# Kernel tuning notes

Measured on AMD Instinct MI355X. Metric: run time of the kernel, lower is better.

## Reference

```python
import jax, jax.numpy as jnp
import numpy as np

N = 10000   # num_nodes (batch=1)
E = 160000  # num edges
CIN, H, T, OUT, K = 32, 64, 12, 12, 3


def _conv1d(x, w, b, pad):
    # x: [N, C_in, T], w: [C_out, C_in, K]
    out = jax.lax.conv_general_dilated(
        x, w, window_strides=(1,), padding=[(pad, pad)],
        dimension_numbers=('NCH', 'OIH', 'NCH'))
    return out + b[None, :, None]


def _gated_tconv(x, w, b):
    # GatedTemporalConv (dropout = identity in eval)
    out = _conv1d(x, w, b, K // 2)
    P, Q = jnp.split(out, 2, axis=1)
    return P * jax.nn.sigmoid(Q)


def _gcn(x, W, b, src, dst, ew):
    # PyG GCNConv, vectorized over all T timesteps in one fused pass.
    # x: [N, C_in, T], W: [C_out, C_in]
    xt = jnp.einsum('nct,oc->not', x, W)
    loop = jnp.arange(N)
    srcl = jnp.concatenate([src, loop])
    dstl = jnp.concatenate([dst, loop])
    ewl = jnp.concatenate([ew, jnp.ones((N,), ew.dtype)])
    deg = jax.ops.segment_sum(ewl, dstl, num_segments=N)
    dis = jnp.where(deg > 0, jax.lax.rsqrt(deg), 0.0)
    norm = dis[srcl] * ewl * dis[dstl]                      # [E+N]
    msg = xt[srcl] * norm[:, None, None]                    # [E+N, C_out, T]
    out = jax.ops.segment_sum(msg, dstl, num_segments=N)    # [N, C_out, T]
    return out + b[None, :, None]


def setup_inputs() -> dict:
    key = jax.random.key(0)
    ks = jax.random.split(key, 20)
    rn = lambda k, s: jax.random.normal(k, s, jnp.float32) * 0.05
    return {
        'x': jax.random.normal(ks[0], (N, CIN, T), jnp.float32),
        'edge_index': jax.random.randint(ks[1], (2, E), 0, N),
        'edge_weight': jax.random.uniform(ks[2], (E,), jnp.float32),
        'tc1a_w': rn(ks[3], (2 * H, CIN, K)), 'tc1a_b': rn(ks[4], (2 * H,)),
        'gc1_w': rn(ks[5], (H, H)),           'gc1_b': rn(ks[6], (H,)),
        'tc1b_w': rn(ks[7], (2 * H, H, K)),   'tc1b_b': rn(ks[8], (2 * H,)),
        'tc2a_w': rn(ks[9], (2 * H, H, K)),   'tc2a_b': rn(ks[10], (2 * H,)),
        'gc2_w': rn(ks[11], (H, H)),          'gc2_b': rn(ks[12], (H,)),
        'tc2b_w': rn(ks[13], (2 * H, H, K)),  'tc2b_b': rn(ks[14], (2 * H,)),
        'fin_w': rn(ks[15], (OUT, H, T)),     'fin_b': rn(ks[16], (OUT,)),
    }


def reference(x, edge_index, edge_weight,
              tc1a_w, tc1a_b, gc1_w, gc1_b, tc1b_w, tc1b_b,
              tc2a_w, tc2a_b, gc2_w, gc2_b, tc2b_w, tc2b_b,
              fin_w, fin_b):
    src, dst = edge_index[0], edge_index[1]
    h = _gated_tconv(x, tc1a_w, tc1a_b)
    h = jax.nn.relu(_gcn(h, gc1_w, gc1_b, src, dst, edge_weight))
    h = _gated_tconv(h, tc1b_w, tc1b_b)
    h = _gated_tconv(h, tc2a_w, tc2a_b)
    h = jax.nn.relu(_gcn(h, gc2_w, gc2_b, src, dst, edge_weight))
    h = _gated_tconv(h, tc2b_w, tc2b_b)
    h = _conv1d(h, fin_w, fin_b, 0)          # [N, OUT, 1] (kernel == T)
    h = h[:, :, 0]                            # squeeze(-1)
    return h.reshape(1, N, OUT)               # batch_size = 1
```

## Files before the change

kernel.cpp:

```cpp
#include <hip/hip_runtime.h>
#include <hip/hip_bf16.h>
#include <stdint.h>

#define N_NODES 10000
#define N_EDGES 160000

typedef unsigned short u16;
typedef unsigned int u32;
typedef short s16v8 __attribute__((ext_vector_type(8)));
typedef float f32v4 __attribute__((ext_vector_type(4)));

__device__ __forceinline__ float bf2f(u16 v){ return __uint_as_float(((u32)v) << 16); }
__device__ __forceinline__ u16 f2bf(float f){
    u32 u = __float_as_uint(f);
    u32 r = (u + 0x7fffu + ((u >> 16) & 1u)) >> 16;
    return (u16)r;
}

struct SmallPtrs { const void* p[14]; };

__device__ __constant__ const int g_seg_off[15] = {
    0, 12288, 12416, 16512, 16576, 41152, 41280,
    65856, 65984, 70080, 70144, 94720, 94848, 104064, 104076
};
__device__ __constant__ const int g_seg_kind[14] = {
    1, 0, 0, 0, 2, 0, 2, 0, 0, 0, 2, 0, 0, 0
};

__global__ void k_convert_init(SmallPtrs ps, u16* __restrict__ dst,
                               float* deg, int* cnt, int* cur){
    int i = blockIdx.x * blockDim.x + threadIdx.x;
    if (i < 104076){
        int seg = 0, base = 0;
#pragma unroll
        for (int s = 0; s < 14; s++){
            if (i >= g_seg_off[s]){ seg = s; base = g_seg_off[s]; }
        }
        int li = i - base;
        float v = ((const float*)ps.p[seg])[li];
        int kind = g_seg_kind[seg];
        int dsto = li;
        if (kind){
            int CIN = (kind == 1) ? 32 : 64;
            int o = li / (3 * CIN);
            int rem = li - o * (3 * CIN);
            int c = rem / 3, d = rem - c * 3;
            dsto = d * 128 * CIN + o * CIN + c;
        }
        dst[base + dsto] = f2bf(v);
    }
    if (i < N_NODES){ deg[i] = 1.0f; cnt[i] = 0; cur[i] = 0; }
}

__launch_bounds__(256, 2)
__global__ void k_gconv_count(const float* __restrict__ xin, const u16* __restrict__ wg,
                              const u16* __restrict__ bg, u16* __restrict__ out,
                              const int* __restrict__ ei, const float* __restrict__ ew,
                              float* deg, int* cnt){
    if (blockIdx.x >= 1250){
        int e = (blockIdx.x - 1250) * 256 + threadIdx.x;
        if (e < N_EDGES){
            int d = ei[N_EDGES + e];
            atomicAdd(&deg[d], ew[e]);
            atomicAdd(&cnt[d], 1);
        }
        return;
    }
    __shared__ __attribute__((aligned(16))) u16 xT[8][14][40];
    __shared__ __attribute__((aligned(16))) u16 Ho[8][12][72];
    int tid = threadIdx.x;
    int n0 = blockIdx.x * 8;

    for (int i = tid; i < 8 * 40; i += 256){
        int g = i / 40, c = i % 40;
        xT[g][0][c] = 0; xT[g][13][c] = 0;
    }
    {
        int g = tid >> 5, c = tid & 31;
        const float4* p = (const float4*)(xin + ((size_t)(n0 + g) * 32 + c) * 12);
        float4 v0 = p[0], v1 = p[1], v2 = p[2];
        xT[g][1][c] = f2bf(v0.x);  xT[g][2][c] = f2bf(v0.y);
        xT[g][3][c] = f2bf(v0.z);  xT[g][4][c] = f2bf(v0.w);
        xT[g][5][c] = f2bf(v1.x);  xT[g][6][c] = f2bf(v1.y);
        xT[g][7][c] = f2bf(v1.z);  xT[g][8][c] = f2bf(v1.w);
        xT[g][9][c] = f2bf(v2.x);  xT[g][10][c] = f2bf(v2.y);
        xT[g][11][c] = f2bf(v2.z); xT[g][12][c] = f2bf(v2.w);
    }
    int lane = tid & 63, wave = tid >> 6;
    int col = lane & 15, quad = lane >> 4;
    int o_p = wave * 16 + col, o_q = o_p + 64;

    s16v8 Bf[3][2];
#pragma unroll
    for (int pq = 0; pq < 2; pq++){
        int o = pq ? o_q : o_p;
#pragma unroll
        for (int d = 0; d < 3; d++)
            Bf[d][pq] = *(const s16v8*)(wg + d * 4096 + o * 32 + quad * 8);
    }
    __syncthreads();

    f32v4 aP[6], aQ[6];
#pragma unroll
    for (int mt = 0; mt < 6; mt++){ aP[mt] = (f32v4)0.f; aQ[mt] = (f32v4)0.f; }
#pragma unroll
    for (int mt = 0; mt < 6; mt++){
        int m = mt * 16 + col;
        int g = m / 12, t = m - 12 * g;
#pragma unroll
        for (int d = 0; d < 3; d++){
            s16v8 a = *(const s16v8*)&xT[g][t + d][quad * 8];
            aP[mt] = __builtin_amdgcn_mfma_f32_16x16x32_bf16(a, Bf[d][0], aP[mt], 0, 0, 0);
            aQ[mt] = __builtin_amdgcn_mfma_f32_16x16x32_bf16(a, Bf[d][1], aQ[mt], 0, 0, 0);
        }
    }
    float bP = bf2f(bg[o_p]), bQ = bf2f(bg[o_q]);
#pragma unroll
    for (int mt = 0; mt < 6; mt++){
#pragma unroll
        for (int r = 0; r < 4; r++){
            int m2 = mt * 16 + quad * 4 + r;
            int g = m2 / 12, t = m2 - 12 * g;
            float pv = aP[mt][r] + bP, qv = aQ[mt][r] + bQ;
            Ho[g][t][o_p] = f2bf(pv / (1.f + __expf(-qv)));
        }
    }
    __syncthreads();
    for (int i = tid; i < 768; i += 256){
        int g = i / 96, r = i % 96, t = r / 8, ch = r % 8;
        *(s16v8*)(out + (size_t)(n0 + g) * 768 + t * 64 + ch * 8) = *(const s16v8*)&Ho[g][t][ch * 8];
    }
}

__global__ void k_scan_dis(const int* __restrict__ cnt, int* __restrict__ off,
                           const float* __restrict__ deg, float* __restrict__ dis){
    __shared__ int wsum[16], woff[16];
    int t = threadIdx.x;
    int lane = t & 63, wv = t >> 6;
    int base = t * 10;
    int loc[10];
    int mysum = 0;
    if (base < N_NODES){
#pragma unroll
        for (int j = 0; j < 10; j++){ loc[j] = mysum; mysum += cnt[base + j]; }
    }
    int s = mysum;
#pragma unroll
    for (int d = 1; d < 64; d <<= 1){
        int v = __shfl_up(s, d, 64);
        if (lane >= d) s += v;
    }
    if (lane == 63) wsum[wv] = s;
    __syncthreads();
    if (t < 16){
        int v = wsum[t];
        int sc = v;
#pragma unroll
        for (int d = 1; d < 16; d <<= 1){
            int u = __shfl_up(sc, d, 16);
            if (t >= d) sc += u;
        }
        woff[t] = sc - v;
        if (t == 15) off[N_NODES] = sc;
    }
    __syncthreads();
    int tbase = woff[wv] + (s - mysum);
    if (base < N_NODES){
#pragma unroll
        for (int j = 0; j < 10; j++) off[base + j] = tbase + loc[j];
    }
    for (int i = t; i < N_NODES; i += 1024) dis[i] = rsqrtf(deg[i]);
}

__global__ void k_scatter(const int* __restrict__ ei, const float* __restrict__ ew,
                          const float* __restrict__ dis, const int* __restrict__ off,
                          int* cur, int2* __restrict__ epack){
    int e = blockIdx.x * blockDim.x + threadIdx.x;
    if (e < N_EDGES){
        int s = ei[e];
        int d = ei[N_EDGES + e];
        float nw = dis[s] * ew[e] * dis[d];
        int p = off[d] + atomicAdd(&cur[d], 1);
        epack[p] = make_int2(s, __float_as_int(nw));
    }
}

#define XIDX(g, row, c) (((g) * 14 + (row)) * 72 + (c))

template<bool LAST>
__launch_bounds__(256, 2)
__global__ void k_fused(const u16* __restrict__ src,
                        const float* __restrict__ dis, const int* __restrict__ off,
                        const int2* __restrict__ ep,
                        const u16* __restrict__ Wmix, const u16* __restrict__ bmix,
                        const u16* __restrict__ w1, const u16* __restrict__ b1,
                        const u16* __restrict__ w2, const u16* __restrict__ b2,
                        const u16* __restrict__ fw, const u16* __restrict__ fb,
                        u16* __restrict__ outMid, float* __restrict__ outFin){
    __shared__ __attribute__((aligned(16))) u16 bufX[8 * 14 * 72];
    __shared__ __attribute__((aligned(16))) u16 bufY[8 * 14 * 72];
    int tid = threadIdx.x;
    int n0 = blockIdx.x * 8;
    int lane = tid & 63, wave = tid >> 6;
    int col = lane & 15, quad = lane >> 4;

    for (int i = tid; i < 8 * 72; i += 256){
        int g = i / 72, c = i % 72;
        bufX[XIDX(g, 0, c)] = 0; bufX[XIDX(g, 13, c)] = 0;
        bufY[XIDX(g, 0, c)] = 0; bufY[XIDX(g, 13, c)] = 0;
    }

    {
        int g = tid >> 5, j = tid & 31;
        int n = n0 + g;
        float dv = dis[n];
        float sw = dv * dv;
        const u16* xr = src + (size_t)n * 768 + j * 24;
        float acc[24];
#pragma unroll
        for (int k = 0; k < 3; k++){
            s16v8 v = *(const s16v8*)(xr + k * 8);
#pragma unroll
            for (int q = 0; q < 8; q++) acc[k * 8 + q] = sw * bf2f((u16)v[q]);
        }
        int b = off[n], e = off[n + 1];
        for (int p = b; p < e; p++){
            int2 pr = ep[p];
            float w = __int_as_float(pr.y);
            const u16* qr = src + (size_t)pr.x * 768 + j * 24;
#pragma unroll
            for (int k = 0; k < 3; k++){
                s16v8 v = *(const s16v8*)(qr + k * 8);
#pragma unroll
                for (int q = 0; q < 8; q++) acc[k * 8 + q] = fmaf(w, bf2f((u16)v[q]), acc[k * 8 + q]);
            }
        }
#pragma unroll
        for (int k = 0; k < 3; k++){
            int flat = j * 24 + k * 8;
            int t = flat >> 6, c = flat & 63;
            s16v8 hv;
#pragma unroll
            for (int q = 0; q < 8; q++) hv[q] = (short)f2bf(acc[k * 8 + q]);
            *(s16v8*)&bufX[XIDX(g, 1 + t, c)] = hv;
        }
    }

    int o_mix = wave * 16 + col;
    s16v8 Bm[2];
#pragma unroll
    for (int ks = 0; ks < 2; ks++)
        Bm[ks] = *(const s16v8*)(Wmix + (size_t)o_mix * 64 + ks * 32 + quad * 8);
    __syncthreads();

    {
        f32v4 accm[6];
#pragma unroll
        for (int mt = 0; mt < 6; mt++) accm[mt] = (f32v4)0.f;
#pragma unroll
        for (int mt = 0; mt < 6; mt++){
            int m = mt * 16 + col;
            int g = m / 12, t = m - 12 * g;
#pragma unroll
            for (int ks = 0; ks < 2; ks++){
                s16v8 a = *(const s16v8*)&bufX[XIDX(g, 1 + t, ks * 32 + quad * 8)];
                accm[mt] = __builtin_amdgcn_mfma_f32_16x16x32_bf16(a, Bm[ks], accm[mt], 0, 0, 0);
            }
        }
        float bm = bf2f(bmix[o_mix]);
#pragma unroll
        for (int mt = 0; mt < 6; mt++){
#pragma unroll
            for (int r = 0; r < 4; r++){
                int m2 = mt * 16 + quad * 4 + r;
                int g = m2 / 12, t = m2 - 12 * g;
                bufY[XIDX(g, 1 + t, o_mix)] = f2bf(fmaxf(accm[mt][r] + bm, 0.f));
            }
        }
    }
    __syncthreads();

    {
        int o_p = wave * 16 + col, o_q = o_p + 64;
        s16v8 Bf[3][2][2];
#pragma unroll
        for (int pq = 0; pq < 2; pq++){
            int o = pq ? o_q : o_p;
#pragma unroll
            for (int d = 0; d < 3; d++)
#pragma unroll
                for (int ks = 0; ks < 2; ks++)
                    Bf[d][ks][pq] = *(const s16v8*)(w1 + d * 8192 + o * 64 + ks * 32 + quad * 8);
        }
        f32v4 aP[6], aQ[6];
#pragma unroll
        for (int mt = 0; mt < 6; mt++){ aP[mt] = (f32v4)0.f; aQ[mt] = (f32v4)0.f; }
#pragma unroll
        for (int mt = 0; mt < 6; mt++){
            int m = mt * 16 + col;
            int g = m / 12, t = m - 12 * g;
#pragma unroll
            for (int d = 0; d < 3; d++)
#pragma unroll
                for (int ks = 0; ks < 2; ks++){
                    s16v8 a = *(const s16v8*)&bufY[XIDX(g, t + d, ks * 32 + quad * 8)];
                    aP[mt] = __builtin_amdgcn_mfma_f32_16x16x32_bf16(a, Bf[d][ks][0], aP[mt], 0, 0, 0);
                    aQ[mt] = __builtin_amdgcn_mfma_f32_16x16x32_bf16(a, Bf[d][ks][1], aQ[mt], 0, 0, 0);
                }
        }
        float bP = bf2f(b1[o_p]), bQ = bf2f(b1[o_q]);
#pragma unroll
        for (int mt = 0; mt < 6; mt++){
#pragma unroll
            for (int r = 0; r < 4; r++){
                int m2 = mt * 16 + quad * 4 + r;
                int g = m2 / 12, t = m2 - 12 * g;
                float pv = aP[mt][r] + bP, qv = aQ[mt][r] + bQ;
                u16 hv = f2bf(pv / (1.f + __expf(-qv)));
                if (LAST) bufX[g * 1008 + o_p * 12 + t] = hv;
                else      bufX[XIDX(g, 1 + t, o_p)] = hv;
            }
        }
    }
    __syncthreads();

    if (!LAST){
        int o_p = wave * 16 + col, o_q = o_p + 64;
        s16v8 Bf[3][2][2];
#pragma unroll
        for (int pq = 0; pq < 2; pq++){
            int o = pq ? o_q : o_p;
#pragma unroll
            for (int d = 0; d < 3; d++)
#pragma unroll
                for (int ks = 0; ks < 2; ks++)
                    Bf[d][ks][pq] = *(const s16v8*)(w2 + d * 8192 + o * 64 + ks * 32 + quad * 8);
        }
        f32v4 aP[6], aQ[6];
#pragma unroll
        for (int mt = 0; mt < 6; mt++){ aP[mt] = (f32v4)0.f; aQ[mt] = (f32v4)0.f; }
#pragma unroll
        for (int mt = 0; mt < 6; mt++){
            int m = mt * 16 + col;
            int g = m / 12, t = m - 12 * g;
#pragma unroll
            for (int d = 0; d < 3; d++)
#pragma unroll
                for (int ks = 0; ks < 2; ks++){
                    s16v8 a = *(const s16v8*)&bufX[XIDX(g, t + d, ks * 32 + quad * 8)];
                    aP[mt] = __builtin_amdgcn_mfma_f32_16x16x32_bf16(a, Bf[d][ks][0], aP[mt], 0, 0, 0);
                    aQ[mt] = __builtin_amdgcn_mfma_f32_16x16x32_bf16(a, Bf[d][ks][1], aQ[mt], 0, 0, 0);
                }
        }
        float bP = bf2f(b2[o_p]), bQ = bf2f(b2[o_q]);
#pragma unroll
        for (int mt = 0; mt < 6; mt++){
#pragma unroll
            for (int r = 0; r < 4; r++){
                int m2 = mt * 16 + quad * 4 + r;
                int g = m2 / 12, t = m2 - 12 * g;
                float pv = aP[mt][r] + bP, qv = aQ[mt][r] + bQ;
                bufY[XIDX(g, 1 + t, o_p)] = f2bf(pv / (1.f + __expf(-qv)));
            }
        }
        __syncthreads();
        for (int i = tid; i < 768; i += 256){
            int g = i / 96, r = i % 96, t = r / 8, ch = r % 8;
            *(s16v8*)(outMid + (size_t)(n0 + g) * 768 + t * 64 + ch * 8) =
                *(const s16v8*)&bufY[XIDX(g, 1 + t, ch * 8)];
        }
    } else {
        if (wave == 0){
            f32v4 accF = {0.f, 0.f, 0.f, 0.f};
            int g8 = col & 7;
#pragma unroll
            for (int ks = 0; ks < 24; ks++){
                s16v8 a = *(const s16v8*)&bufX[g8 * 1008 + ks * 32 + quad * 8];
                s16v8 bfr = {0, 0, 0, 0, 0, 0, 0, 0};
                if (col < 12)
                    bfr = *(const s16v8*)(fw + (size_t)col * 768 + ks * 32 + quad * 8);
                accF = __builtin_amdgcn_mfma_f32_16x16x32_bf16(a, bfr, accF, 0, 0, 0);
            }
            if (col < 12){
                float bb = bf2f(fb[col]);
#pragma unroll
                for (int r = 0; r < 4; r++){
                    int g = quad * 4 + r;
                    if (g < 8) outFin[(size_t)(n0 + g) * 12 + col] = accF[r] + bb;
                }
            }
        }
    }
}

static inline size_t align256(size_t x){ return (x + 255) & ~(size_t)255; }

extern "C" void kernel_launch(void* const* d_in, const int* in_sizes, int n_in,
                              void* d_out, int out_size, void* d_ws, size_t ws_size,
                              hipStream_t stream){
    const float* x  = (const float*)d_in[0];
    const int* ei   = (const int*)d_in[1];
    const float* ew = (const float*)d_in[2];

    char* w = (char*)d_ws;
    u16* bufA    = (u16*)w;  w += align256((size_t)N_NODES * 768 * sizeof(u16));
    u16* bufB    = (u16*)w;  w += align256((size_t)N_NODES * 768 * sizeof(u16));
    float* deg   = (float*)w; w += align256(N_NODES * sizeof(float));
    float* dis   = (float*)w; w += align256(N_NODES * sizeof(float));
    int* cnt     = (int*)w;   w += align256(N_NODES * sizeof(int));
    int* off     = (int*)w;   w += align256((N_NODES + 1) * sizeof(int));
    int* cur     = (int*)w;   w += align256(N_NODES * sizeof(int));
    int2* epack  = (int2*)w;  w += align256((size_t)N_EDGES * sizeof(int2));
    u16* cvt     = (u16*)w;   w += align256(104076 * sizeof(u16));

    u16* tc1a_w = cvt + 0;
    u16* tc1a_b = cvt + 12288;
    u16* gc1_w  = cvt + 12416;
    u16* gc1_b  = cvt + 16512;
    u16* tc1b_w = cvt + 16576;
    u16* tc1b_b = cvt + 41152;
    u16* tc2a_w = cvt + 41280;
    u16* tc2a_b = cvt + 65856;
    u16* gc2_w  = cvt + 65984;
    u16* gc2_b  = cvt + 70080;
    u16* tc2b_w = cvt + 70144;
    u16* tc2b_b = cvt + 94720;
    u16* fin_w  = cvt + 94848;
    u16* fin_b  = cvt + 104064;

    SmallPtrs ps;
    ps.p[0]  = d_in[3];  ps.p[1]  = d_in[4];
    ps.p[2]  = d_in[5];  ps.p[3]  = d_in[6];
    ps.p[4]  = d_in[7];  ps.p[5]  = d_in[8];
    ps.p[6]  = d_in[9];  ps.p[7]  = d_in[10];
    ps.p[8]  = d_in[11]; ps.p[9]  = d_in[12];
    ps.p[10] = d_in[13]; ps.p[11] = d_in[14];
    ps.p[12] = d_in[15]; ps.p[13] = d_in[16];

    k_convert_init<<<(104076 + 255) / 256, 256, 0, stream>>>(ps, cvt, deg, cnt, cur);
    k_gconv_count<<<1250 + 625, 256, 0, stream>>>(x, tc1a_w, tc1a_b, bufA, ei, ew, deg, cnt);
    k_scan_dis<<<1, 1024, 0, stream>>>(cnt, off, deg, dis);
    k_scatter<<<625, 256, 0, stream>>>(ei, ew, dis, off, cur, epack);

    k_fused<false><<<1250, 256, 0, stream>>>(bufA, dis, off, epack,
                                             gc1_w, gc1_b, tc1b_w, tc1b_b,
                                             tc2a_w, tc2a_b, nullptr, nullptr,
                                             bufB, nullptr);
    k_fused<true><<<1250, 256, 0, stream>>>(bufB, dis, off, epack,
                                            gc2_w, gc2_b, tc2b_w, tc2b_b,
                                            nullptr, nullptr, fin_w, fin_b,
                                            nullptr, (float*)d_out);
}
```

Measured before the change: 266.6 us.

## Halve nodes per block, gather with a full wave per node, raise occupancy

Each fused block now handles 4 nodes instead of 8, and the grid doubles to 2500 blocks. The GCN gather assigns one 64-lane wave per node with coalesced 8-byte loads, unrolled two edges at a time. Launch bounds rise to 6 blocks per CU. The aim is more parallelism and memory-level concurrency in the latency-bound neighbour gather. The cost is fewer MFMA tiles per block, since weight fragments are reloaded per block for half as many rows, and possible register pressure from the higher occupancy target.

Result: faster. 254.6 us (-4.5%).

```diff
diff --git a/kernel.cpp b/kernel.cpp
--- a/kernel.cpp
+++ b/kernel.cpp
@@ -188,7 +188,7 @@
 #define XIDX(g, row, c) (((g) * 14 + (row)) * 72 + (c))
 
 template<bool LAST>
-__launch_bounds__(256, 2)
+__launch_bounds__(256, 6)
 __global__ void k_fused(const u16* __restrict__ src,
                         const float* __restrict__ dis, const int* __restrict__ off,
                         const int2* __restrict__ ep,
@@ -197,52 +197,82 @@
                         const u16* __restrict__ w2, const u16* __restrict__ b2,
                         const u16* __restrict__ fw, const u16* __restrict__ fb,
                         u16* __restrict__ outMid, float* __restrict__ outFin){
-    __shared__ __attribute__((aligned(16))) u16 bufX[8 * 14 * 72];
-    __shared__ __attribute__((aligned(16))) u16 bufY[8 * 14 * 72];
+    __shared__ __attribute__((aligned(16))) u16 bufX[4 * 14 * 72];
+    __shared__ __attribute__((aligned(16))) u16 bufY[4 * 14 * 72];
     int tid = threadIdx.x;
-    int n0 = blockIdx.x * 8;
+    int n0 = blockIdx.x * 4;
     int lane = tid & 63, wave = tid >> 6;
     int col = lane & 15, quad = lane >> 4;
 
-    for (int i = tid; i < 8 * 72; i += 256){
+    for (int i = tid; i < 4 * 72; i += 256){
         int g = i / 72, c = i % 72;
         bufX[XIDX(g, 0, c)] = 0; bufX[XIDX(g, 13, c)] = 0;
         bufY[XIDX(g, 0, c)] = 0; bufY[XIDX(g, 13, c)] = 0;
     }
 
     {
-        int g = tid >> 5, j = tid & 31;
+        int g = wave, j = lane;
         int n = n0 + g;
         float dv = dis[n];
         float sw = dv * dv;
-        const u16* xr = src + (size_t)n * 768 + j * 24;
-        float acc[24];
-#pragma unroll
-        for (int k = 0; k < 3; k++){
-            s16v8 v = *(const s16v8*)(xr + k * 8);
-#pragma unroll
-            for (int q = 0; q < 8; q++) acc[k * 8 + q] = sw * bf2f((u16)v[q]);
+        int j4 = j * 4;
+        const u16* xr = src + (size_t)n * 768 + j4;
+        float acc[12];
+#pragma unroll
+        for (int i = 0; i < 3; i++){
+            ushort4 v = *(const ushort4*)(xr + i * 256);
+            acc[i * 4 + 0] = sw * bf2f(v.x);
+            acc[i * 4 + 1] = sw * bf2f(v.y);
+            acc[i * 4 + 2] = sw * bf2f(v.z);
+            acc[i * 4 + 3] = sw * bf2f(v.w);
         }
         int b = off[n], e = off[n + 1];
-        for (int p = b; p < e; p++){
-            int2 pr = ep[p];
-            float w = __int_as_float(pr.y);
-            const u16* qr = src + (size_t)pr.x * 768 + j * 24;
-#pragma unroll
-            for (int k = 0; k < 3; k++){
-                s16v8 v = *(const s16v8*)(qr + k * 8);
-#pragma unroll
-                for (int q = 0; q < 8; q++) acc[k * 8 + q] = fmaf(w, bf2f((u16)v[q]), acc[k * 8 + q]);
-            }
-        }
-#pragma unroll
-        for (int k = 0; k < 3; k++){
-            int flat = j * 24 + k * 8;
-            int t = flat >> 6, c = flat & 63;
-            s16v8 hv;
-#pragma unroll
-            for (int q = 0; q < 8; q++) hv[q] = (short)f2bf(acc[k * 8 + q]);
-            *(s16v8*)&bufX[XIDX(g, 1 + t, c)] = hv;
+        int p = b;
+        for (; p + 1 < e; p += 2){
+            int2 e0 = ep[p], e1 = ep[p + 1];
+            float w0 = __int_as_float(e0.y), w1v = __int_as_float(e1.y);
+            const u16* q0 = src + (size_t)e0.x * 768 + j4;
+            const u16* q1 = src + (size_t)e1.x * 768 + j4;
+            ushort4 a0 = *(const ushort4*)(q0);
+            ushort4 a1 = *(const ushort4*)(q0 + 256);
+            ushort4 a2 = *(const ushort4*)(q0 + 512);
+            ushort4 c0 = *(const ushort4*)(q1);
+            ushort4 c1 = *(const ushort4*)(q1 + 256);
+            ushort4 c2 = *(const ushort4*)(q1 + 512);
+            acc[0] = fmaf(w0, bf2f(a0.x), acc[0]); acc[1] = fmaf(w0, bf2f(a0.y), acc[1]);
+            acc[2] = fmaf(w0, bf2f(a0.z), acc[2]); acc[3] = fmaf(w0, bf2f(a0.w), acc[3]);
+            acc[4] = fmaf(w0, bf2f(a1.x), acc[4]); acc[5] = fmaf(w0, bf2f(a1.y), acc[5]);
+            acc[6] = fmaf(w0, bf2f(a1.z), acc[6]); acc[7] = fmaf(w0, bf2f(a1.w), acc[7]);
+            acc[8] = fmaf(w0, bf2f(a2.x), acc[8]); acc[9] = fmaf(w0, bf2f(a2.y), acc[9]);
+            acc[10] = fmaf(w0, bf2f(a2.z), acc[10]); acc[11] = fmaf(w0, bf2f(a2.w), acc[11]);
+            acc[0] = fmaf(w1v, bf2f(c0.x), acc[0]); acc[1] = fmaf(w1v, bf2f(c0.y), acc[1]);
+            acc[2] = fmaf(w1v, bf2f(c0.z), acc[2]); acc[3] = fmaf(w1v, bf2f(c0.w), acc[3]);
+            acc[4] = fmaf(w1v, bf2f(c1.x), acc[4]); acc[5] = fmaf(w1v, bf2f(c1.y), acc[5]);
+            acc[6] = fmaf(w1v, bf2f(c1.z), acc[6]); acc[7] = fmaf(w1v, bf2f(c1.w), acc[7]);
+            acc[8] = fmaf(w1v, bf2f(c2.x), acc[8]); acc[9] = fmaf(w1v, bf2f(c2.y), acc[9]);
+            acc[10] = fmaf(w1v, bf2f(c2.z), acc[10]); acc[11] = fmaf(w1v, bf2f(c2.w), acc[11]);
+        }
+        if (p < e){
+            int2 e0 = ep[p];
+            float w0 = __int_as_float(e0.y);
+            const u16* q0 = src + (size_t)e0.x * 768 + j4;
+#pragma unroll
+            for (int i = 0; i < 3; i++){
+                ushort4 v = *(const ushort4*)(q0 + i * 256);
+                acc[i * 4 + 0] = fmaf(w0, bf2f(v.x), acc[i * 4 + 0]);
+                acc[i * 4 + 1] = fmaf(w0, bf2f(v.y), acc[i * 4 + 1]);
+                acc[i * 4 + 2] = fmaf(w0, bf2f(v.z), acc[i * 4 + 2]);
+                acc[i * 4 + 3] = fmaf(w0, bf2f(v.w), acc[i * 4 + 3]);
+            }
+        }
+        int t0 = j >> 4, c = j4 & 63;
+#pragma unroll
+        for (int i = 0; i < 3; i++){
+            int t = t0 + i * 4;
+            ushort4 hv;
+            hv.x = f2bf(acc[i * 4 + 0]); hv.y = f2bf(acc[i * 4 + 1]);
+            hv.z = f2bf(acc[i * 4 + 2]); hv.w = f2bf(acc[i * 4 + 3]);
+            *(ushort4*)&bufX[XIDX(g, 1 + t, c)] = hv;
         }
     }
 
@@ -254,11 +284,11 @@
     __syncthreads();
 
     {
-        f32v4 accm[6];
-#pragma unroll
-        for (int mt = 0; mt < 6; mt++) accm[mt] = (f32v4)0.f;
-#pragma unroll
-        for (int mt = 0; mt < 6; mt++){
+        f32v4 accm[3];
+#pragma unroll
+        for (int mt = 0; mt < 3; mt++) accm[mt] = (f32v4)0.f;
+#pragma unroll
+        for (int mt = 0; mt < 3; mt++){
             int m = mt * 16 + col;
             int g = m / 12, t = m - 12 * g;
 #pragma unroll
@@ -269,7 +299,7 @@
         }
         float bm = bf2f(bmix[o_mix]);
 #pragma unroll
-        for (int mt = 0; mt < 6; mt++){
+        for (int mt = 0; mt < 3; mt++){
 #pragma unroll
             for (int r = 0; r < 4; r++){
                 int m2 = mt * 16 + quad * 4 + r;
@@ -292,11 +322,11 @@
                 for (int ks = 0; ks < 2; ks++)
                     Bf[d][ks][pq] = *(const s16v8*)(w1 + d * 8192 + o * 64 + ks * 32 + quad * 8);
         }
-        f32v4 aP[6], aQ[6];
-#pragma unroll
-        for (int mt = 0; mt < 6; mt++){ aP[mt] = (f32v4)0.f; aQ[mt] = (f32v4)0.f; }
-#pragma unroll
-        for (int mt = 0; mt < 6; mt++){
+        f32v4 aP[3], aQ[3];
+#pragma unroll
+        for (int mt = 0; mt < 3; mt++){ aP[mt] = (f32v4)0.f; aQ[mt] = (f32v4)0.f; }
+#pragma unroll
+        for (int mt = 0; mt < 3; mt++){
             int m = mt * 16 + col;
             int g = m / 12, t = m - 12 * g;
 #pragma unroll
@@ -310,7 +340,7 @@
         }
         float bP = bf2f(b1[o_p]), bQ = bf2f(b1[o_q]);
 #pragma unroll
-        for (int mt = 0; mt < 6; mt++){
+        for (int mt = 0; mt < 3; mt++){
 #pragma unroll
             for (int r = 0; r < 4; r++){
                 int m2 = mt * 16 + quad * 4 + r;
@@ -336,11 +366,11 @@
                 for (int ks = 0; ks < 2; ks++)
                     Bf[d][ks][pq] = *(const s16v8*)(w2 + d * 8192 + o * 64 + ks * 32 + quad * 8);
         }
-        f32v4 aP[6], aQ[6];
-#pragma unroll
-        for (int mt = 0; mt < 6; mt++){ aP[mt] = (f32v4)0.f; aQ[mt] = (f32v4)0.f; }
-#pragma unroll
-        for (int mt = 0; mt < 6; mt++){
+        f32v4 aP[3], aQ[3];
+#pragma unroll
+        for (int mt = 0; mt < 3; mt++){ aP[mt] = (f32v4)0.f; aQ[mt] = (f32v4)0.f; }
+#pragma unroll
+        for (int mt = 0; mt < 3; mt++){
             int m = mt * 16 + col;
             int g = m / 12, t = m - 12 * g;
 #pragma unroll
@@ -354,7 +384,7 @@
         }
         float bP = bf2f(b2[o_p]), bQ = bf2f(b2[o_q]);
 #pragma unroll
-        for (int mt = 0; mt < 6; mt++){
+        for (int mt = 0; mt < 3; mt++){
 #pragma unroll
             for (int r = 0; r < 4; r++){
                 int m2 = mt * 16 + quad * 4 + r;
@@ -364,7 +394,7 @@
             }
         }
         __syncthreads();
-        for (int i = tid; i < 768; i += 256){
+        for (int i = tid; i < 384; i += 256){
             int g = i / 96, r = i % 96, t = r / 8, ch = r % 8;
             *(s16v8*)(outMid + (size_t)(n0 + g) * 768 + t * 64 + ch * 8) =
                 *(const s16v8*)&bufY[XIDX(g, 1 + t, ch * 8)];
@@ -372,21 +402,21 @@
     } else {
         if (wave == 0){
             f32v4 accF = {0.f, 0.f, 0.f, 0.f};
-            int g8 = col & 7;
+            int g4 = col & 3;
 #pragma unroll
             for (int ks = 0; ks < 24; ks++){
-                s16v8 a = *(const s16v8*)&bufX[g8 * 1008 + ks * 32 + quad * 8];
+                s16v8 a = *(const s16v8*)&bufX[g4 * 1008 + ks * 32 + quad * 8];
                 s16v8 bfr = {0, 0, 0, 0, 0, 0, 0, 0};
                 if (col < 12)
                     bfr = *(const s16v8*)(fw + (size_t)col * 768 + ks * 32 + quad * 8);
                 accF = __builtin_amdgcn_mfma_f32_16x16x32_bf16(a, bfr, accF, 0, 0, 0);
             }
-            if (col < 12){
+            if (col < 12 && quad == 0){
                 float bb = bf2f(fb[col]);
 #pragma unroll
                 for (int r = 0; r < 4; r++){
-                    int g = quad * 4 + r;
-                    if (g < 8) outFin[(size_t)(n0 + g) * 12 + col] = accF[r] + bb;
+                    int g = r;
+                    outFin[(size_t)(n0 + g) * 12 + col] = accF[r] + bb;
                 }
             }
         }
@@ -442,11 +472,11 @@
     k_scan_dis<<<1, 1024, 0, stream>>>(cnt, off, deg, dis);
     k_scatter<<<625, 256, 0, stream>>>(ei, ew, dis, off, cur, epack);
 
-    k_fused<false><<<1250, 256, 0, stream>>>(bufA, dis, off, epack,
+    k_fused<false><<<2500, 256, 0, stream>>>(bufA, dis, off, epack,
                                              gc1_w, gc1_b, tc1b_w, tc1b_b,
                                              tc2a_w, tc2a_b, nullptr, nullptr,
                                              bufB, nullptr);
-    k_fused<true><<<1250, 256, 0, stream>>>(bufB, dis, off, epack,
+    k_fused<true><<<2500, 256, 0, stream>>>(bufB, dis, off, epack,
                                             gc2_w, gc2_b, tc2b_w, tc2b_b,
                                             nullptr, nullptr, fin_w, fin_b,
                                             nullptr, (float*)d_out);
```
